# Performance work log

Hardware: AMD Instinct MI355X
Metric: run time of the kernel (lower is better)

Reference implementation:

```python
import jax, jax.numpy as jnp
import numpy as np

D_MODEL = 1024
NUM_HEADS = 16
HEAD_DIM = D_MODEL // NUM_HEADS
B, S = 2, 2048


def setup_inputs() -> dict:
    key = jax.random.key(0)
    ks = jax.random.split(key, 12)
    s = 1.0 / np.sqrt(D_MODEL)
    return {
        "query": jax.random.normal(ks[0], (B, S, D_MODEL), jnp.float32),
        "key": jax.random.normal(ks[1], (B, S, D_MODEL), jnp.float32),
        "value": jax.random.normal(ks[2], (B, S, D_MODEL), jnp.float32),
        "attn_mask": jnp.ones((B, 1, 1, S), dtype=bool),
        "w_q": jax.random.uniform(ks[3], (D_MODEL, D_MODEL), jnp.float32, -s, s),
        "b_q": jax.random.uniform(ks[4], (D_MODEL,), jnp.float32, -s, s),
        "w_k": jax.random.uniform(ks[5], (D_MODEL, D_MODEL), jnp.float32, -s, s),
        "b_k": jax.random.uniform(ks[6], (D_MODEL,), jnp.float32, -s, s),
        "w_v": jax.random.uniform(ks[7], (D_MODEL, D_MODEL), jnp.float32, -s, s),
        "b_v": jax.random.uniform(ks[8], (D_MODEL,), jnp.float32, -s, s),
        "w_o": jax.random.uniform(ks[9], (D_MODEL, D_MODEL), jnp.float32, -s, s),
        "b_o": jax.random.uniform(ks[10], (D_MODEL,), jnp.float32, -s, s),
    }


def _split_heads(x):
    b, s, _ = x.shape
    return x.reshape(b, s, NUM_HEADS, HEAD_DIM).transpose(0, 2, 1, 3)  # [B,H,S,hd]


def reference(query, key, value, attn_mask, w_q, b_q, w_k, b_k, w_v, b_v, w_o, b_o):
    q = _split_heads(query @ w_q.T + b_q)
    k = _split_heads(key @ w_k.T + b_k)
    v = _split_heads(value @ w_v.T + b_v)
    scale = 1.0 / np.sqrt(HEAD_DIM).astype(np.float32)
    scores = jnp.einsum("bhqd,bhkd->bhqk", q, k) * scale  # [B,H,S,S]
    scores = jnp.where(attn_mask, scores, jnp.float32(-1e9))
    weights = jax.nn.softmax(scores, axis=-1)
    attended = jnp.einsum("bhqk,bhkd->bhqd", weights, v)
    merged = attended.transpose(0, 2, 1, 3).reshape(query.shape[0], query.shape[1], D_MODEL)
    return merged @ w_o.T + b_o
```

## Files before the change

### kernel.cpp

```cpp
#include <hip/hip_runtime.h>

#define D_MODEL 1024
#define NHEADS 16
#define HDIM 64
#define BATCH 2
#define SEQ 2048

typedef __attribute__((ext_vector_type(8))) short short8;
typedef __attribute__((ext_vector_type(4))) float floatx4;

__device__ __forceinline__ short f2bf(float f) {
    unsigned u = __builtin_bit_cast(unsigned, f);
    u += 0x7fffu + ((u >> 16) & 1u);
    return (short)(u >> 16);
}

#if defined(__has_builtin)
#if __has_builtin(__builtin_amdgcn_cvt_pk_bf16_f32)
#define HAS_PK_BF16 1
#endif
#if __has_builtin(__builtin_amdgcn_exp2f)
#define EXP2(x) __builtin_amdgcn_exp2f(x)
#endif
#endif
#ifndef EXP2
#define EXP2(x) exp2f(x)
#endif
__device__ __forceinline__ unsigned pk2bf(float a, float b) {
#ifdef HAS_PK_BF16
    auto r = __builtin_amdgcn_cvt_pk_bf16_f32(a, b);
    unsigned out;
    __builtin_memcpy(&out, &r, 4);
    return out;
#else
    unsigned ua = __builtin_bit_cast(unsigned, a);
    ua += 0x7fffu + ((ua >> 16) & 1u);
    unsigned ub = __builtin_bit_cast(unsigned, b);
    ub += 0x7fffu + ((ub >> 16) & 1u);
    return (ua >> 16) | (ub & 0xffff0000u);
#endif
}

__device__ __forceinline__ void gll16(const void* g, void* l) {
    __builtin_amdgcn_global_load_lds(
        (const __attribute__((address_space(1))) unsigned int*)g,
        (__attribute__((address_space(3))) unsigned int*)l, 16, 0, 0);
}

__global__ __launch_bounds__(256)
void cvt_all(const float* __restrict__ q, const float* __restrict__ k,
             const float* __restrict__ v, const float* __restrict__ wq,
             const float* __restrict__ wk, const float* __restrict__ wv,
             const float* __restrict__ wo, short* __restrict__ ws)
{
    const int seg = blockIdx.y;
    const float* src; short* dst; int n;
    const int M4 = 1 << 22, M1 = 1 << 20;
    switch (seg) {
        case 0: src = q;  dst = ws;                    n = M4; break;
        case 1: src = k;  dst = ws + M4;               n = M4; break;
        case 2: src = v;  dst = ws + 2 * M4;           n = M4; break;
        case 3: src = wq; dst = ws + 3 * M4;           n = M1; break;
        case 4: src = wk; dst = ws + 3 * M4 + M1;      n = M1; break;
        case 5: src = wv; dst = ws + 3 * M4 + 2 * M1;  n = M1; break;
        default:src = wo; dst = ws + 3 * M4 + 3 * M1;  n = M1; break;
    }
    int idx = (blockIdx.x * 256 + threadIdx.x) * 8;
    if (idx >= n) return;
    float4 f0 = *(const float4*)(src + idx);
    float4 f1 = *(const float4*)(src + idx + 4);
    uint4 o = { pk2bf(f0.x, f0.y), pk2bf(f0.z, f0.w),
                pk2bf(f1.x, f1.y), pk2bf(f1.z, f1.w) };
    *(uint4*)(dst + idx) = o;
}

template<int FINAL>
__global__ __launch_bounds__(256)
void gemm_pipe(const short* __restrict__ Abase, const short* __restrict__ Wbase,
               const float* __restrict__ b0, const float* __restrict__ b1,
               const float* __restrict__ b2, void* __restrict__ outp,
               float scale0)
{
    constexpr int BM = FINAL ? 64 : 128;
    constexpr int WM = FINAL ? 32 : 64;
    constexpr int MT = WM / 16;
    constexpr int AG = BM / 32;
    __shared__ short smem[BM * 64 + 128 * 64];
    short* As = smem;
    short* Bs = smem + BM * 64;

    const int tid  = threadIdx.x;
    const int lane = tid & 63;
    const int w    = tid >> 6;
    const int wr   = (w >> 1) * WM;
    const int wc   = (w & 1) * 64;
    const int m0   = blockIdx.y * BM;
    const int n0   = blockIdx.x * 128;
    const int z    = FINAL ? 0 : blockIdx.z;

    const short* A = Abase + (size_t)z * (1 << 22);
    const short* W = Wbase + (size_t)z * (1 << 20);
    const float* bias = FINAL ? b0 : (z == 0 ? b0 : (z == 1 ? b1 : b2));
    const float scale = (!FINAL && z == 0) ? scale0 : 1.0f;

    const int slr = lane >> 3;
    const int scb = (lane & 7) ^ slr;
    const int fm  = lane & 15;
    const int fq  = lane >> 4;

    const short* aSrc[AG];
    const short* bSrc[4];
#pragma unroll
    for (int i = 0; i < AG; ++i)
        aSrc[i] = A + (size_t)(m0 + (w * AG + i) * 8 + slr) * D_MODEL + scb * 8;
#pragma unroll
    for (int i = 0; i < 4; ++i)
        bSrc[i] = W + (size_t)(n0 + (w * 4 + i) * 8 + slr) * D_MODEL + scb * 8;

    short8 pa[AG], pb[4];
#pragma unroll
    for (int i = 0; i < AG; ++i) pa[i] = *(const short8*)(aSrc[i]);
#pragma unroll
    for (int i = 0; i < 4; ++i)  pb[i] = *(const short8*)(bSrc[i]);

    floatx4 acc[MT][4] = {};

    for (int k0 = 0; k0 < D_MODEL; k0 += 64) {
        __syncthreads();
#pragma unroll
        for (int i = 0; i < AG; ++i)
            *(short8*)(As + (w * AG + i) * 512 + lane * 8) = pa[i];
#pragma unroll
        for (int i = 0; i < 4; ++i)
            *(short8*)(Bs + (w * 4 + i) * 512 + lane * 8) = pb[i];
        const int kn = (k0 + 64) & (D_MODEL - 1);
#pragma unroll
        for (int i = 0; i < AG; ++i) pa[i] = *(const short8*)(aSrc[i] + kn);
#pragma unroll
        for (int i = 0; i < 4; ++i)  pb[i] = *(const short8*)(bSrc[i] + kn);
        __syncthreads();

#pragma unroll
        for (int ks = 0; ks < 2; ++ks) {
            short8 af[MT], bfv[4];
#pragma unroll
            for (int mt = 0; mt < MT; ++mt) {
                int row = wr + mt * 16 + fm;
                af[mt] = *(const short8*)(As + row * 64 + ((ks * 4 + fq) ^ (row & 7)) * 8);
            }
#pragma unroll
            for (int nt = 0; nt < 4; ++nt) {
                int row = wc + nt * 16 + fm;
                bfv[nt] = *(const short8*)(Bs + row * 64 + ((ks * 4 + fq) ^ (row & 7)) * 8);
            }
#pragma unroll
            for (int mt = 0; mt < MT; ++mt)
#pragma unroll
                for (int nt = 0; nt < 4; ++nt)
                    acc[mt][nt] = __builtin_amdgcn_mfma_f32_16x16x32_bf16(
                        af[mt], bfv[nt], acc[mt][nt], 0, 0, 0);
        }
    }

    if (!FINAL && z == 2) {
        __syncthreads();
        short* T = smem;
#pragma unroll
        for (int nt = 0; nt < 4; ++nt) {
            int nl = wc + nt * 16 + fm;
            float bv = bias[n0 + nl];
#pragma unroll
            for (int mt = 0; mt < MT; ++mt)
#pragma unroll
                for (int r = 0; r < 4; ++r) {
                    int m = wr + mt * 16 + fq * 4 + r;
                    int mp = (m & 64) | ((m & 15) << 2) | ((m >> 4) & 3);
                    T[nl * 128 + (((mp >> 3) ^ (nl & 15)) << 3) + (mp & 7)]
                        = f2bf(acc[mt][nt][r] + bv);
                }
        }
        __syncthreads();
        const int nl   = tid >> 1, half = tid & 1;
        const int gb   = m0 >> 11;
        const int gh   = (n0 + nl) >> 6, gd = (n0 + nl) & 63;
        const int ms   = m0 & 2047;
        short* gdst = (short*)outp + ((size_t)2 << 22)
                    + ((((size_t)(gb * NHEADS + gh)) << 6) + gd) * SEQ + ms;
#pragma unroll
        for (int c = 0; c < 8; ++c) {
            int lc = half * 8 + c;
            int p  = lc ^ (nl & 15);
            *(short8*)(gdst + lc * 8) = *(const short8*)(T + nl * 128 + p * 8);
        }
        return;
    }
#pragma unroll
    for (int nt = 0; nt < 4; ++nt) {
        int n = n0 + wc + nt * 16 + fm;
        float bv = bias[n];
#pragma unroll
        for (int mt = 0; mt < MT; ++mt) {
#pragma unroll
            for (int r = 0; r < 4; ++r) {
                int m = m0 + wr + mt * 16 + fq * 4 + r;
                float val = (acc[mt][nt][r] + bv) * scale;
                if (FINAL) {
                    ((float*)outp)[(size_t)m * D_MODEL + n] = val;
                } else {
                    short* outz = (short*)outp + (size_t)z * (1 << 22);
                    int b = m >> 11, s = m & 2047, h = n >> 6, d = n & 63;
                    outz[(((size_t)(b * NHEADS + h) * SEQ + s) << 6) + d] = f2bf(val);
                }
            }
        }
    }
}

__global__ __launch_bounds__(256)
void flash5(const short* __restrict__ qh, const short* __restrict__ kh,
            const short* __restrict__ vT, short* __restrict__ ab)
{
    __shared__ short Ks[2 * 64 * 64];
    __shared__ short Vt[2 * 64 * 64];
    __shared__ short Ps[64 * 64];

    const int tid  = threadIdx.x;
    const int lane = tid & 63;
    const int w    = tid >> 6;
    const int wq0  = w * 16;
    const int bh   = blockIdx.y;
    const int b    = bh >> 4, h = bh & 15;
    const int s0   = blockIdx.x * 64;
    const size_t base = (size_t)bh << 17;

    const int fm = lane & 15;
    const int fq = lane >> 4;
    const int fk = fq * 8;

    short8 qf[2];
#pragma unroll
    for (int ks = 0; ks < 2; ++ks)
        qf[ks] = *(const short8*)(qh + base +
            (size_t)(s0 + wq0 + fm) * HDIM + ks * 32 + fk);

    const int slr = lane >> 3;
    const int lcb = (lane & 7) ^ slr;

    const short8 ones = { 0x3f80, 0x3f80, 0x3f80, 0x3f80,
                          0x3f80, 0x3f80, 0x3f80, 0x3f80 };

    floatx4 O[4] = {};
    floatx4 accL = {};

    for (int kt = 0; kt < SEQ; kt += 128) {
        __syncthreads();
#pragma unroll
        for (int sub = 0; sub < 2; ++sub) {
#pragma unroll
            for (int i = 0; i < 2; ++i) {
                int g = w * 2 + i;
                int row = g * 8 + slr;
                gll16(kh + base + (size_t)(kt + sub * 64 + row) * HDIM + lcb * 8,
                      Ks + sub * 4096 + g * 512);
                gll16(vT + base + (size_t)row * SEQ + kt + sub * 64 + lcb * 8,
                      Vt + sub * 4096 + g * 512);
            }
        }
        __syncthreads();

#pragma unroll
        for (int sub = 0; sub < 2; ++sub) {
            const short* Kb = Ks + sub * 4096;
            const short* Vb = Vt + sub * 4096;

            floatx4 sc[4] = {};
#pragma unroll
            for (int ks = 0; ks < 2; ++ks) {
                short8 bfv[4];
#pragma unroll
                for (int nt = 0; nt < 4; ++nt) {
                    int row = nt * 16 + fm;
                    bfv[nt] = *(const short8*)(Kb + row * 64 + ((ks * 4 + fq) ^ (row & 7)) * 8);
                }
#pragma unroll
                for (int nt = 0; nt < 4; ++nt)
                    sc[nt] = __builtin_amdgcn_mfma_f32_16x16x32_bf16(
                        qf[ks], bfv[nt], sc[nt], 0, 0, 0);
            }

#pragma unroll
            for (int r = 0; r < 4; ++r) {
                float p0 = EXP2(sc[0][r]);
                float p1 = EXP2(sc[1][r]);
                float p2 = EXP2(sc[2][r]);
                float p3 = EXP2(sc[3][r]);
                int row = wq0 + fq * 4 + r;
                uint2 pv = { pk2bf(p0, p1), pk2bf(p2, p3) };
                *(uint2*)(Ps + row * 64 + (((fm >> 1) ^ (row & 7)) << 3) + ((fm & 1) << 2)) = pv;
            }

#pragma unroll
            for (int ks = 0; ks < 2; ++ks) {
                int arow = wq0 + fm;
                short8 af = *(const short8*)(Ps + arow * 64 + ((ks * 4 + fq) ^ (arow & 7)) * 8);
                short8 bfv[4];
#pragma unroll
                for (int nt = 0; nt < 4; ++nt) {
                    int d = nt * 16 + fm;
                    bfv[nt] = *(const short8*)(Vb + d * 64 + ((ks * 4 + fq) ^ (d & 7)) * 8);
                }
                accL = __builtin_amdgcn_mfma_f32_16x16x32_bf16(af, ones, accL, 0, 0, 0);
#pragma unroll
                for (int nt = 0; nt < 4; ++nt)
                    O[nt] = __builtin_amdgcn_mfma_f32_16x16x32_bf16(
                        af, bfv[nt], O[nt], 0, 0, 0);
            }
        }
    }

#pragma unroll
    for (int r = 0; r < 4; ++r) {
        float inv = 1.0f / accL[r];
        int s = s0 + wq0 + fq * 4 + r;
        short* orow = ab + (((size_t)(b * SEQ + s) * NHEADS + h) << 6);
#pragma unroll
        for (int nt = 0; nt < 4; ++nt)
            orow[nt * 16 + fm] = f2bf(O[nt][r] * inv);
    }
}

extern "C" void kernel_launch(void* const* d_in, const int* in_sizes, int n_in,
                              void* d_out, int out_size, void* d_ws, size_t ws_size,
                              hipStream_t stream) {
    const float* query = (const float*)d_in[0];
    const float* key_  = (const float*)d_in[1];
    const float* value = (const float*)d_in[2];
    const float* bq = (const float*)d_in[5];
    const float* bk = (const float*)d_in[7];
    const float* bv = (const float*)d_in[9];
    const float* bo = (const float*)d_in[11];
    float* out = (float*)d_out;

    const int M4 = 1 << 22, M1 = 1 << 20;
    short* ws  = (short*)d_ws;
    short* qx  = ws;
    short* wqb = ws + 3 * M4;
    short* wob = wqb + 3 * M1;
    short* qh  = ws + 4 * M4;
    short* khd = ws + 5 * M4;
    short* vTh = ws + 6 * M4;
    short* ab  = ws + 7 * M4;

    const float SCALE = 0.125f * 1.44269504088896340736f;

    dim3 blk(256);
    cvt_all<<<dim3(2048, 7), blk, 0, stream>>>(
        query, key_, value, (const float*)d_in[4], (const float*)d_in[6],
        (const float*)d_in[8], (const float*)d_in[10], ws);

    gemm_pipe<0><<<dim3(D_MODEL / 128, (BATCH * SEQ) / 128, 3), blk, 0, stream>>>(
        qx, wqb, bq, bk, bv, qh, SCALE);

    flash5<<<dim3(SEQ / 64, BATCH * NHEADS), blk, 0, stream>>>(qh, khd, vTh, ab);

    gemm_pipe<1><<<dim3(D_MODEL / 128, (BATCH * SEQ) / 64), blk, 0, stream>>>(
        ab, wob, bo, bo, bo, out, 1.0f);
}
```

Measured before the change: 231.9 us.

## Vectorize GEMM and attention epilogue stores via permuted head-dim layout

Q/K projection and attention outputs are now written as packed 4-bf16 vectors, using a permuted head-dim order (d -> (d%16)*4 + d/16). The output weight w_o is converted to bf16 with its columns permuted the same way so the final GEMM stays consistent. The final GEMM stages its fp32 tile through swizzled shared memory and writes coalesced float4 rows. The goal is to replace scattered 2-byte and 4-byte global stores with wide coalesced ones, at the cost of extra shared-memory traffic and strided scalar stores during the w_o conversion.

```diff
diff --git a/kernel.cpp b/kernel.cpp
--- a/kernel.cpp
+++ b/kernel.cpp
@@ -67,6 +67,16 @@
     }
     int idx = (blockIdx.x * 256 + threadIdx.x) * 8;
     if (idx >= n) return;
+    if (seg == 6) {
+        int row = idx >> 10, d0 = idx & 63;
+        short* drow = dst + row * 1024 + ((idx & 1023) & ~63);
+        int base = ((d0 & 15) << 2) | (d0 >> 4);
+        const float* s = src + idx;
+#pragma unroll
+        for (int i = 0; i < 8; ++i)
+            drow[base + i * 4] = f2bf(s[i]);
+        return;
+    }
     float4 f0 = *(const float4*)(src + idx);
     float4 f1 = *(const float4*)(src + idx + 4);
     uint4 o = { pk2bf(f0.x, f0.y), pk2bf(f0.z, f0.w),
@@ -85,7 +95,9 @@
     constexpr int WM = FINAL ? 32 : 64;
     constexpr int MT = WM / 16;
     constexpr int AG = BM / 32;
-    __shared__ short smem[BM * 64 + 128 * 64];
+    constexpr int STG = BM * 64 + 128 * 64;
+    constexpr int SME = (STG > (FINAL ? 16384 : 0)) ? STG : 16384;
+    __shared__ short smem[SME];
     short* As = smem;
     short* Bs = smem + BM * 64;
 
@@ -162,7 +174,34 @@
         }
     }
 
-    if (!FINAL && z == 2) {
+    if (FINAL) {
+        __syncthreads();
+        float* T = (float*)smem;
+#pragma unroll
+        for (int nt = 0; nt < 4; ++nt) {
+            int nl = wc + nt * 16 + fm;
+            float bv = bias[n0 + nl];
+            int c = nl >> 2, wd = nl & 3;
+#pragma unroll
+            for (int mt = 0; mt < MT; ++mt)
+#pragma unroll
+                for (int r = 0; r < 4; ++r) {
+                    int ml = wr + mt * 16 + fq * 4 + r;
+                    T[ml * 128 + ((c ^ (fq << 3)) << 2) + wd] = acc[mt][nt][r] + bv;
+                }
+        }
+        __syncthreads();
+#pragma unroll
+        for (int it = 0; it < 8; ++it) {
+            int o  = it * 1024 + tid * 4;
+            int ml = o >> 7, nl = o & 127;
+            int fqv = (ml >> 2) & 3;
+            float4 v = *(const float4*)&T[ml * 128 + (((nl >> 2) ^ (fqv << 3)) << 2)];
+            *(float4*)&((float*)outp)[(size_t)(m0 + ml) * D_MODEL + n0 + nl] = v;
+        }
+        return;
+    }
+    if (z == 2) {
         __syncthreads();
         short* T = smem;
 #pragma unroll
@@ -194,23 +233,26 @@
         }
         return;
     }
-#pragma unroll
-    for (int nt = 0; nt < 4; ++nt) {
-        int n = n0 + wc + nt * 16 + fm;
-        float bv = bias[n];
+    {
+        short* outz = (short*)outp + (size_t)z * (1 << 22);
+        const int head = (n0 + wc) >> 6;
+        float bvs[4];
+#pragma unroll
+        for (int nt = 0; nt < 4; ++nt)
+            bvs[nt] = bias[n0 + wc + nt * 16 + fm];
 #pragma unroll
         for (int mt = 0; mt < MT; ++mt) {
 #pragma unroll
             for (int r = 0; r < 4; ++r) {
                 int m = m0 + wr + mt * 16 + fq * 4 + r;
-                float val = (acc[mt][nt][r] + bv) * scale;
-                if (FINAL) {
-                    ((float*)outp)[(size_t)m * D_MODEL + n] = val;
-                } else {
-                    short* outz = (short*)outp + (size_t)z * (1 << 22);
-                    int b = m >> 11, s = m & 2047, h = n >> 6, d = n & 63;
-                    outz[(((size_t)(b * NHEADS + h) * SEQ + s) << 6) + d] = f2bf(val);
-                }
+                int b = m >> 11, s = m & 2047;
+                float v0 = (acc[mt][0][r] + bvs[0]) * scale;
+                float v1 = (acc[mt][1][r] + bvs[1]) * scale;
+                float v2 = (acc[mt][2][r] + bvs[2]) * scale;
+                float v3 = (acc[mt][3][r] + bvs[3]) * scale;
+                uint2 pv = { pk2bf(v0, v1), pk2bf(v2, v3) };
+                *(uint2*)(outz + (((size_t)(b * NHEADS + head) * SEQ + s) << 6)
+                          + fm * 4) = pv;
             }
         }
     }
@@ -323,9 +365,9 @@
         float inv = 1.0f / accL[r];
         int s = s0 + wq0 + fq * 4 + r;
         short* orow = ab + (((size_t)(b * SEQ + s) * NHEADS + h) << 6);
-#pragma unroll
-        for (int nt = 0; nt < 4; ++nt)
-            orow[nt * 16 + fm] = f2bf(O[nt][r] * inv);
+        uint2 pv = { pk2bf(O[0][r] * inv, O[1][r] * inv),
+                     pk2bf(O[2][r] * inv, O[3][r] * inv) };
+        *(uint2*)(orow + fm * 4) = pv;
     }
 }
 
```

Result: slower. 238.9 us (+3.0%).
